# Kernel tuning notes

Measured on AMD Instinct MI355X. Metric: run time of the kernel, lower is better.

## Reference

```python
import jax, jax.numpy as jnp
import numpy as np

STRIDES = (128, 64, 32, 16, 8)
FM_SHAPES = ((6, 10), (12, 20), (24, 40), (48, 80), (96, 160))
RATIOS = np.array([1.0, 2.0, 3.0])
BASE_SIZE = 4
POS_THR, NEG_THR, IGNORE = 0.5, 0.4, -1.0
ALPHA, GAMMA, SIGMA = 0.25, 2.0, 3.0


def _cell_anchors(stride):
    # classic generate_anchors: base 4x4 anchor, 3 aspect ratios, scale=stride
    w = h = float(BASE_SIZE)
    ctr = (BASE_SIZE - 1) / 2.0
    size = w * h
    ws = np.round(np.sqrt(size / RATIOS))
    hs = np.round(ws * RATIOS)
    a = np.stack([ctr - 0.5 * (ws - 1), ctr - 0.5 * (hs - 1),
                  ctr + 0.5 * (ws - 1), ctr + 0.5 * (hs - 1)], 1)
    aw = a[:, 2] - a[:, 0] + 1
    ah = a[:, 3] - a[:, 1] + 1
    cx = a[:, 0] + 0.5 * (aw - 1)
    cy = a[:, 1] + 0.5 * (ah - 1)
    sw = aw * stride
    sh = ah * stride
    return np.stack([cx - 0.5 * (sw - 1), cy - 0.5 * (sh - 1),
                     cx + 0.5 * (sw - 1), cy + 0.5 * (sh - 1)], 1)


def _all_anchors():
    outs = []
    for (h, w), s in zip(FM_SHAPES, STRIDES):
        cell = _cell_anchors(s)  # [3,4]
        sx = np.tile((np.arange(w) * s)[None, :], (h, 1)).reshape(-1)
        sy = np.tile((np.arange(h) * s)[:, None], (1, w)).reshape(-1)
        shifts = np.stack([sx, sy, sx, sy], 1)  # [h*w,4]
        outs.append((cell[None] + shifts[:, None]).reshape(-1, 4))
    return np.concatenate(outs, 0).astype(np.float32)  # [A,4]


def box_overlap(b, g):
    ab = (b[:, 2] - b[:, 0] + 1) * (b[:, 3] - b[:, 1] + 1)
    ag = (g[:, 2] - g[:, 0] + 1) * (g[:, 3] - g[:, 1] + 1)
    iw = jnp.clip(jnp.minimum(b[:, None, 2], g[None, :, 2]) - jnp.maximum(b[:, None, 0], g[None, :, 0]) + 1, 0)
    ih = jnp.clip(jnp.minimum(b[:, None, 3], g[None, :, 3]) - jnp.maximum(b[:, None, 1], g[None, :, 1]) + 1, 0)
    inter = iw * ih
    return inter / (ab[:, None] + ag[None, :] - inter)


def bbox_transform_inv(anc, dlt):
    w = anc[..., 2] - anc[..., 0] + 1
    h = anc[..., 3] - anc[..., 1] + 1
    cx = anc[..., 0] + 0.5 * (w - 1)
    cy = anc[..., 1] + 0.5 * (h - 1)
    mx = jnp.log(jnp.asarray(1000.0 / 16, dlt.dtype))
    pw = jnp.exp(jnp.minimum(dlt[..., 2], mx)) * w
    ph = jnp.exp(jnp.minimum(dlt[..., 3], mx)) * h
    pcx = dlt[..., 0] * w + cx
    pcy = dlt[..., 1] * h + cy
    return jnp.stack([pcx - 0.5 * (pw - 1), pcy - 0.5 * (ph - 1),
                      pcx + 0.5 * (pw - 1), pcy + 0.5 * (ph - 1)], -1)


def bbox_transform(anc, gt):
    aw = anc[..., 2] - anc[..., 0] + 1
    ah = anc[..., 3] - anc[..., 1] + 1
    acx = anc[..., 0] + 0.5 * (aw - 1)
    acy = anc[..., 1] + 0.5 * (ah - 1)
    gw = gt[..., 2] - gt[..., 0] + 1
    gh = gt[..., 3] - gt[..., 1] + 1
    gcx = gt[..., 0] + 0.5 * (gw - 1)
    gcy = gt[..., 1] + 0.5 * (gh - 1)
    return jnp.stack([(gcx - acx) / aw, (gcy - acy) / ah,
                      jnp.log(gw / aw), jnp.log(gh / ah)], -1)


def conv3x3(x, w, b):
    y = jax.lax.conv_general_dilated(x, w, (1, 1), 'SAME',
                                     dimension_numbers=('NCHW', 'OIHW', 'NCHW'))
    return y + b[None, :, None, None]


def _head(feat, cls_w, cls_b, box_w, box_b, score_w, score_b,
          bpred_w, bpred_b, iou_w, iou_b, num_w, num_b):
    n = feat.shape[0]
    c = feat
    for i in range(4):
        c = jax.nn.relu(conv3x3(c, cls_w[i], cls_b[i]))
    cls_prob = jax.nn.sigmoid(conv3x3(c, score_w, score_b))
    num_prob = conv3x3(c, num_w, num_b)
    r = feat
    for i in range(4):
        r = jax.nn.relu(conv3x3(r, box_w[i], box_b[i]))
    offsets = conv3x3(r, bpred_w, bpred_b)
    iou_prob = conv3x3(r, iou_w, iou_b)
    rs = lambda t, ch: t.transpose(0, 2, 3, 1).reshape(n, -1, ch)
    return rs(cls_prob, 2), rs(num_prob, 2), rs(offsets, 8), rs(iou_prob, 2)


def _forward(feats, gt_boxes, im_info, cls_w, cls_b, box_w, box_b,
             score_w, score_b, bpred_w, bpred_b, iou_w, iou_b, num_w, num_b):
    outs = [_head(f, cls_w, cls_b, box_w, box_b, score_w, score_b,
                  bpred_w, bpred_b, iou_w, iou_b, num_w, num_b) for f in feats]
    cls_prob = jnp.concatenate([o[0] for o in outs], 1)  # [n,A,2]
    num_prob = jnp.concatenate([o[1] for o in outs], 1)  # [n,A,2]
    offsets = jnp.concatenate([o[2] for o in outs], 1)   # [n,A,8]
    iou_prob = jnp.concatenate([o[3] for o in outs], 1)  # [n,A,2]
    anchors = jnp.asarray(_all_anchors())                # [A,4]
    A = anchors.shape[0]
    n = cls_prob.shape[0]
    G = gt_boxes.shape[1]
    counts = im_info[:, 5]
    gidx = jnp.arange(G, dtype=jnp.float32)

    def anchor_target_one(gt, cnt):
        valid = (gidx < cnt) & (gt[:, 4] != IGNORE)
        ov = jnp.where(valid[None, :], box_overlap(anchors, gt[:, :4]), -1.0)
        top2, idx = jax.lax.top_k(ov, 2)  # [A,2]
        labels = jnp.where(top2 >= POS_THR, 1.0,
                           jnp.where(top2 < NEG_THR, 0.0, -1.0))
        tgt = bbox_transform(anchors[:, None, :], gt[idx, :4])  # [A,2,4]
        return labels, tgt.reshape(-1, 4)

    rpn_labels, target_boxes = jax.vmap(anchor_target_one)(gt_boxes, counts)
    rpn_labels = jax.lax.stop_gradient(rpn_labels)        # [n,A,2]
    target_boxes = jax.lax.stop_gradient(target_boxes)    # [n,2A,4]
    anchors2 = jnp.repeat(anchors, 2, axis=0)             # [2A,4] interleaved

    def iou_target_one(gt, cnt, off):
        dt = bbox_transform_inv(anchors2, off.reshape(-1, 4))  # [2A,4]
        keep = ((gidx < cnt) & (gt[:, 4] != IGNORE)).astype(dt.dtype)
        ov = box_overlap(dt, gt[:, :4]) * keep[None, :]        # [2A,G]
        ov = ov.reshape(A, 2, G)
        a, b = ov[:, 0], ov[:, 1]
        i1 = jnp.argmax(a, 1)
        av = jnp.take_along_axis(a, i1[:, None], 1)
        b = b.at[jnp.arange(A), i1].set(0.0)
        bv = jnp.max(b, 1, keepdims=True)
        return jnp.concatenate([av, bv], 1)                    # [A,2]

    ious_target = jax.lax.stop_gradient(
        jax.vmap(iou_target_one)(gt_boxes, counts, offsets))

    a, b = rpn_labels[..., 0], rpn_labels[..., 1]
    ignores = b - (a == 0).astype(b.dtype) * (b != 0).astype(b.dtype)
    labels = jnp.stack([a, ignores], 2).reshape(n, -1)     # [n,2A]

    # focal (sigmoid_cross_entropy_retina)
    p = cls_prob.reshape(n, -1, 1)                          # [n,2A,1]
    mask = (labels != IGNORE).astype(p.dtype)
    onehot = ((labels * mask) == 1).astype(p.dtype)[..., None]
    pos = (1 - p) ** GAMMA * onehot * jnp.log(p)
    neg = p ** GAMMA * (1 - onehot) * jnp.log(1 - p)
    npos = jnp.maximum((labels > 0).astype(p.dtype).sum(), 1.0)
    cls_loss = (-(ALPHA * pos + (1 - ALPHA) * neg).sum(-1) * mask).sum() / npos

    # smooth_l1_loss_retina (sigma=3)
    off4 = offsets.reshape(n, -1, 4)                        # [n,2A,4]
    diff = off4 - target_boxes
    ad = jnp.abs(diff)
    s2 = SIGMA * SIGMA
    sl1 = jnp.where(ad < 1.0 / s2, 0.5 * s2 * diff * diff, ad - 0.5 / s2)
    posm = (labels > 0).astype(off4.dtype)
    bbox_loss = (sl1.sum(-1) * posm).sum() / jnp.maximum(posm.sum(), 1.0)

    # iou_l1_loss
    lab2 = labels.reshape(n, -1, 2)                         # [n,A,2]
    ioumask = (lab2 > 0).astype(iou_prob.dtype)
    iou_loss = (jnp.abs(iou_prob.reshape(n, -1, 2) - ious_target) * ioumask).sum() \
        / jnp.maximum(ioumask.sum(), 1.0)

    # softmax_loss over num-per-anchor predictions
    nlabels = (lab2 > 0).sum(2).reshape(-1) - 1             # [n*A] in {-1,0,1}
    score = num_prob.reshape(-1, 2)
    logp = jax.nn.log_softmax(score, -1)
    nm = (nlabels != -1)
    vl = jnp.where(nm, nlabels, 0)
    nmf = nm.astype(score.dtype)
    num_loss = (-(jnp.take_along_axis(logp, vl[:, None], 1)[:, 0]) * nmf).sum() \
        / jnp.maximum(nmf.sum(), 1.0)

    return jnp.stack([cls_loss, 2.0 * bbox_loss, 2.0 * iou_loss, num_loss])


def setup_inputs() -> dict:
    key = jax.random.key(0)
    ks = jax.random.split(key, 24)
    n, G = 2, 32
    inp = {}
    for i, (h, w) in enumerate(FM_SHAPES):
        inp[f"feat_p{7 - i}"] = jax.random.normal(ks[i], (n, 256, h, w), jnp.float32) * 0.5
    x1 = jax.random.uniform(ks[5], (n, G), minval=0.0, maxval=900.0)
    y1 = jax.random.uniform(ks[6], (n, G), minval=0.0, maxval=500.0)
    bw = jax.random.uniform(ks[7], (n, G), minval=32.0, maxval=300.0)
    bh = jax.random.uniform(ks[8], (n, G), minval=32.0, maxval=300.0)
    inp["gt_boxes"] = jnp.stack([x1, y1, x1 + bw, y1 + bh, jnp.ones((n, G))], -1).astype(jnp.float32)
    inp["im_info"] = jnp.tile(jnp.array([[768., 1280., 1., 768., 1280., 24.]], jnp.float32), (n, 1))
    std = 0.01
    inp["cls_w"] = jax.random.normal(ks[9], (4, 256, 256, 3, 3), jnp.float32) * std
    inp["cls_b"] = jnp.zeros((4, 256), jnp.float32)
    inp["box_w"] = jax.random.normal(ks[10], (4, 256, 256, 3, 3), jnp.float32) * std
    inp["box_b"] = jnp.zeros((4, 256), jnp.float32)
    prior_bias = -float(np.log((1 - 0.01) / 0.01))
    inp["score_w"] = jax.random.normal(ks[11], (6, 256, 3, 3), jnp.float32) * std
    inp["score_b"] = jnp.full((6,), prior_bias, jnp.float32)
    inp["bpred_w"] = jax.random.normal(ks[12], (24, 256, 3, 3), jnp.float32) * std
    inp["bpred_b"] = jnp.zeros((24,), jnp.float32)
    inp["iou_w"] = jax.random.normal(ks[13], (6, 256, 3, 3), jnp.float32) * std
    inp["iou_b"] = jnp.zeros((6,), jnp.float32)
    inp["num_w"] = jax.random.normal(ks[14], (6, 256, 3, 3), jnp.float32) * std
    inp["num_b"] = jnp.zeros((6,), jnp.float32)
    return inp


def reference(feat_p7, feat_p6, feat_p5, feat_p4, feat_p3, gt_boxes, im_info,
              cls_w, cls_b, box_w, box_b, score_w, score_b, bpred_w, bpred_b,
              iou_w, iou_b, num_w, num_b):
    feats = [feat_p7, feat_p6, feat_p5, feat_p4, feat_p3]
    return _forward(feats, gt_boxes, im_info, cls_w, cls_b, box_w, box_b,
                    score_w, score_b, bpred_w, bpred_b, iou_w, iou_b, num_w, num_b)
```

## Files before the change

### kernel.cpp

```cpp
#include <hip/hip_runtime.h>
#include <math.h>

#define A_TOTAL 61380
#define NGT 32

typedef _Float16 f16;
typedef f16 f16x8 __attribute__((ext_vector_type(8)));
typedef float f32x4 __attribute__((ext_vector_type(4)));

__device__ __constant__ int LV_H[5]    = {6, 12, 24, 48, 96};
__device__ __constant__ int LV_W[5]    = {10, 20, 40, 80, 160};
__device__ __constant__ int LV_BASE[5] = {0, 60, 300, 1260, 5100};
__device__ __constant__ int LV_TX[5]   = {1, 2, 3, 5, 10};

typedef __attribute__((address_space(1))) const void* gptr_t;
typedef __attribute__((address_space(3))) void* lptr_t;
__device__ __forceinline__ void cp16_g2l(const void* g, void* l) {
  __builtin_amdgcn_global_load_lds((gptr_t)g, (lptr_t)l, 16, 0, 0);
}

__device__ __forceinline__ void get_tile8(int t, int& lv, int& y0, int& x0)
{
  int local;
  if (t >= 44)      { lv = 4; local = t - 44; }
  else if (t >= 14) { lv = 3; local = t - 14; }
  else if (t >= 5)  { lv = 2; local = t - 5; }
  else if (t >= 1)  { lv = 1; local = t - 1; }
  else              { lv = 0; local = 0; }
  int tX = LV_TX[lv];
  y0 = (local / tX) * 8;
  x0 = (local % tX) * 16;
}

__device__ __forceinline__ void get_tile16(int t, int& lv, int& y0, int& x0)
{
  int local;
  if (t >= 24)      { lv = 4; local = t - 24; }
  else if (t >= 9)  { lv = 3; local = t - 9; }
  else if (t >= 3)  { lv = 2; local = t - 3; }
  else if (t >= 1)  { lv = 1; local = t - 1; }
  else              { lv = 0; local = 0; }
  int tX = LV_TX[lv];
  y0 = (local / tX) * 16;
  x0 = (local % tX) * 16;
}

__global__ __launch_bounds__(256) void feats_to_nhwc(
    const float* __restrict__ f0, const float* __restrict__ f1,
    const float* __restrict__ f2, const float* __restrict__ f3,
    const float* __restrict__ f4, f16* __restrict__ act)
{
  const int b = blockIdx.z;
  const int c0 = blockIdx.y * 32;
  const int p0 = blockIdx.x * 32;
  const int tx = threadIdx.x & 31, ty = threadIdx.x >> 5;
  __shared__ float tl[32][33];

  int p = p0 + tx;
  const float* src = f0; int po = 0, HW = 60;
  if (p >= 5100)      { src = f4; po = p - 5100; HW = 15360; }
  else if (p >= 1260) { src = f3; po = p - 1260; HW = 3840; }
  else if (p >= 300)  { src = f2; po = p - 300;  HW = 960; }
  else if (p >= 60)   { src = f1; po = p - 60;   HW = 240; }
  else                { src = f0; po = p;        HW = 60; }

#pragma unroll
  for (int k = 0; k < 4; ++k) {
    int c = c0 + ty + k * 8;
    float v = 0.f;
    if (p < 20460) v = src[((size_t)b * 256 + c) * HW + po];
    tl[ty + k * 8][tx] = v;
  }
  __syncthreads();
#pragma unroll
  for (int k = 0; k < 4; ++k) {
    int pp = p0 + ty + k * 8;
    if (pp < 20460)
      act[((size_t)b * 20460 + pp) * 256 + c0 + tx] = (f16)tl[tx][ty + k * 8];
  }
}

__global__ __launch_bounds__(256) void prep_tower_w3(
    const float* __restrict__ cls_w, const float* __restrict__ box_w,
    f16* __restrict__ wT)
{
  int blk = blockIdx.x;
  int l = blk >> 8, co = blk & 255;
  const float* src = (l < 4 ? cls_w + (size_t)l * 589824
                            : box_w + (size_t)(l - 4) * 589824)
                   + (size_t)co * 2304;
  __shared__ f16 sm[2304];
  int t = threadIdx.x;
#pragma unroll
  for (int j = 0; j < 9; ++j) sm[t + j * 256] = (f16)src[t + j * 256];
  __syncthreads();
#pragma unroll
  for (int it = 0; it < 2; ++it) {
    int c = t + it * 256;
    if (c < 288) {
      int tap = c >> 5, s = c & 31;
      f16x8 v;
#pragma unroll
      for (int e = 0; e < 8; ++e) v[e] = sm[(s * 8 + e) * 9 + tap];
      *(f16x8*)(wT + ((((size_t)l * 9 + tap) * 32 + s) * 256 + co) * 8) = v;
    }
  }
}

__global__ void prep_head_w3(const float* __restrict__ sw, const float* __restrict__ nw,
                             const float* __restrict__ bw, const float* __restrict__ iw,
                             const float* __restrict__ sb, const float* __restrict__ nb2,
                             const float* __restrict__ bb, const float* __restrict__ ib,
                             f16* __restrict__ wH, float* __restrict__ hb)
{
  int idx = blockIdx.x * 256 + threadIdx.x;
  if (idx < 18432) {
    int p = idx / 9216, rem = idx - p * 9216;
    int tap = rem / 1024, rem2 = rem - tap * 1024;
    int s = rem2 >> 5, co = rem2 & 31;
    int C1 = p ? 24 : 6;
    const float* w1 = p ? bw : sw;
    const float* w2 = p ? iw : nw;
    f16x8 v;
#pragma unroll
    for (int e = 0; e < 8; ++e) {
      int ci = s * 8 + e;
      float x = 0.f;
      if (co < C1)          x = w1[((size_t)co * 256 + ci) * 9 + tap];
      else if (co < C1 + 6) x = w2[((size_t)(co - C1) * 256 + ci) * 9 + tap];
      v[e] = (f16)x;
    }
    *(f16x8*)(wH + (size_t)idx * 8) = v;
  }
  if (idx < 64) {
    int pp = idx >> 5, jj = idx & 31;
    int C1b = pp ? 24 : 6;
    const float* b1 = pp ? bb : sb;
    const float* b2 = pp ? ib : nb2;
    float bv = 0.f;
    if (jj < C1b)          bv = b1[jj];
    else if (jj < C1b + 6) bv = b2[jj - C1b];
    hb[idx] = bv;
  }
}

__global__ __launch_bounds__(256, 2) void conv_mfma_tower2(
    const f16* __restrict__ in_cls, f16* __restrict__ out_cls,
    const f16* __restrict__ in_box, f16* __restrict__ out_box,
    const f16* __restrict__ wT, const float* __restrict__ cls_b,
    const float* __restrict__ box_b, int layer)
{
  int lv, y0, x0;
  get_tile8(blockIdx.x, lv, y0, x0);
  const int H = LV_H[lv], W = LV_W[lv], base = LV_BASE[lv];
  const int b = blockIdx.y, tw = blockIdx.z;
  const f16* in  = tw ? in_box : in_cls;
  f16*       out = tw ? out_box : out_cls;
  const f16* wB = wT + (size_t)(tw * 4 + layer) * 2304 * 256;
  const float* bias = (tw ? box_b : cls_b) + layer * 256;

  const int tid = threadIdx.x;
  const int lane = tid & 63, wid = tid >> 6;
  const int m = lane & 15, q = lane >> 4;
  const int mrow = (wid & 1) * 4;
  const int ncol = (wid >> 1) * 128;

  __shared__ __align__(16) f16 Al[720 * 8];
  __shared__ __align__(16) f16 Bl[2 * 1024 * 8];

  f32x4 acc[4][8];
#pragma unroll
  for (int i = 0; i < 4; ++i)
#pragma unroll
    for (int j = 0; j < 8; ++j) acc[i][j] = (f32x4){0.f, 0.f, 0.f, 0.f};

  const f16* inb = in + (size_t)(b * 20460 + base) * 256;

  auto stageA = [&](int cb) {
#pragma unroll
    for (int it = 0; it < 3; ++it) {
      int u = tid + it * 256;
      if (u < 720) {
        int r = u / 72, rem = u - r * 72;
        int seg = rem / 18, px = rem - seg * 18;
        int gy = y0 - 1 + r, gx = x0 - 1 + px;
        uint4 v = {0, 0, 0, 0};
        if (gy >= 0 && gy < H && gx >= 0 && gx < W)
          v = *(const uint4*)(inb + (size_t)(gy * W + gx) * 256 + cb * 32 + seg * 8);
        *(uint4*)(Al + (size_t)u * 8) = v;
      }
    }
  };
  auto prefetchB = [&](int cb, int tap, int bsel) {
    const f16* wsrc = wB + (((size_t)tap * 32 + cb * 4) * 256) * 8;
    f16* dst = Bl + (size_t)bsel * 1024 * 8;
#pragma unroll
    for (int it = 0; it < 4; ++it) {
      int u = tid + it * 256;
      cp16_g2l(wsrc + (size_t)u * 8, dst + (size_t)u * 8);
    }
  };

  prefetchB(0, 0, 0);
  int buf = 0;
  for (int cb = 0; cb < 8; ++cb) {
    __syncthreads();
    stageA(cb);
    for (int tap = 0; tap < 9; ++tap) {
      __syncthreads();
      {
        int ncb = cb, ntap = tap + 1;
        if (ntap == 9) { ntap = 0; ncb++; }
        if (ncb < 8) prefetchB(ncb, ntap, buf ^ 1);
      }
      const int ky = tap / 3, kx = tap - ky * 3;
      f16x8 af[4];
#pragma unroll
      for (int mb = 0; mb < 4; ++mb)
        af[mb] = *(const f16x8*)(Al + (size_t)(((mrow + mb + ky) * 4 + q) * 18 + m + kx) * 8);
#pragma unroll
      for (int half = 0; half < 2; ++half) {
        f16x8 bf[4];
#pragma unroll
        for (int nb = 0; nb < 4; ++nb)
          bf[nb] = *(const f16x8*)(Bl + (size_t)(buf * 1024 + q * 256 + ncol + half * 64 + nb * 16 + m) * 8);
#pragma unroll
        for (int mb = 0; mb < 4; ++mb)
#pragma unroll
          for (int nb = 0; nb < 4; ++nb)
            acc[mb][half * 4 + nb] =
                __builtin_amdgcn_mfma_f32_16x16x32_f16(af[mb], bf[nb], acc[mb][half * 4 + nb], 0, 0, 0);
      }
      buf ^= 1;
    }
  }

#pragma unroll
  for (int mb = 0; mb < 4; ++mb) {
    int y = y0 + mrow + mb;
    if (y >= H) continue;
#pragma unroll
    for (int nb = 0; nb < 8; ++nb) {
      int co = ncol + nb * 16 + m;
      float bi = bias[co];
#pragma unroll
      for (int r = 0; r < 4; ++r) {
        int x = x0 + q * 4 + r;
        if (x < W) {
          float v = fmaxf(acc[mb][nb][r] + bi, 0.f);
          out[(size_t)(b * 20460 + base + y * W + x) * 256 + co] = (f16)v;
        }
      }
    }
  }
}

__global__ __launch_bounds__(256) void conv_mfma_head2(
    const f16* __restrict__ in_cls, const f16* __restrict__ in_box,
    const f16* __restrict__ wH, const float* __restrict__ hb,
    float* __restrict__ cls_prob, float* __restrict__ num_prob,
    float* __restrict__ offsets, float* __restrict__ iou_prob)
{
  int lv, y0, x0;
  get_tile16(blockIdx.x, lv, y0, x0);
  const int H = LV_H[lv], W = LV_W[lv], base = LV_BASE[lv];
  const int b = blockIdx.y, z = blockIdx.z;
  const f16* in = z ? in_box : in_cls;
  const f16* wB = wH + (size_t)z * 2304 * 32;
  const float* hbz = hb + z * 32;
  float* o1 = z ? offsets : cls_prob;
  float* o2 = z ? iou_prob : num_prob;
  const int C1 = z ? 24 : 6, P1 = z ? 8 : 2, SIG = z ? 0 : 1;

  const int tid = threadIdx.x;
  const int lane = tid & 63, wid = tid >> 6;
  const int m = lane & 15, q = lane >> 4;

  __shared__ __align__(16) f16 Al[1296 * 8];
  __shared__ __align__(16) f16 Bl[2 * 128 * 8];

  f32x4 acc[4][2];
#pragma unroll
  for (int i = 0; i < 4; ++i) { acc[i][0] = (f32x4){0,0,0,0}; acc[i][1] = (f32x4){0,0,0,0}; }

  const f16* inb = in + (size_t)(b * 20460 + base) * 256;

  auto prefetchB = [&](int cb, int tap, int bsel) {
    if (tid < 128) {
      const f16* wsrc = wB + (((size_t)tap * 32 + cb * 4) * 32) * 8;
      cp16_g2l(wsrc + (size_t)tid * 8, Bl + (size_t)(bsel * 128 + tid) * 8);
    }
  };

  prefetchB(0, 0, 0);
  int buf = 0;
  for (int cb = 0; cb < 8; ++cb) {
    __syncthreads();
#pragma unroll
    for (int it = 0; it < 6; ++it) {
      int u = tid + it * 256;
      if (u < 1296) {
        int r = u / 72, rem = u - r * 72;
        int seg = rem / 18, px = rem - seg * 18;
        int gy = y0 - 1 + r, gx = x0 - 1 + px;
        uint4 v = {0, 0, 0, 0};
        if (gy >= 0 && gy < H && gx >= 0 && gx < W)
          v = *(const uint4*)(inb + (size_t)(gy * W + gx) * 256 + cb * 32 + seg * 8);
        *(uint4*)(Al + (size_t)u * 8) = v;
      }
    }
    for (int tap = 0; tap < 9; ++tap) {
      __syncthreads();
      {
        int ncb = cb, ntap = tap + 1;
        if (ntap == 9) { ntap = 0; ncb++; }
        if (ncb < 8) prefetchB(ncb, ntap, buf ^ 1);
      }
      const int ky = tap / 3, kx = tap - ky * 3;
      f16x8 af[4], bf[2];
#pragma unroll
      for (int mb = 0; mb < 4; ++mb)
        af[mb] = *(const f16x8*)(Al + (size_t)(((wid * 4 + mb + ky) * 4 + q) * 18 + m + kx) * 8);
#pragma unroll
      for (int nb = 0; nb < 2; ++nb)
        bf[nb] = *(const f16x8*)(Bl + (size_t)(buf * 128 + q * 32 + nb * 16 + m) * 8);
#pragma unroll
      for (int mb = 0; mb < 4; ++mb)
#pragma unroll
        for (int nb = 0; nb < 2; ++nb)
          acc[mb][nb] = __builtin_amdgcn_mfma_f32_16x16x32_f16(af[mb], bf[nb], acc[mb][nb], 0, 0, 0);
      buf ^= 1;
    }
  }

  const int ro = base * 3;
#pragma unroll
  for (int mb = 0; mb < 4; ++mb) {
    int y = y0 + wid * 4 + mb;
    if (y >= H) continue;
#pragma unroll
    for (int nb = 0; nb < 2; ++nb) {
      int j = nb * 16 + m;
      if (j >= C1 + 6) continue;
      float bi = hbz[j];
#pragma unroll
      for (int r = 0; r < 4; ++r) {
        int x = x0 + q * 4 + r;
        if (x < W) {
          float v = acc[mb][nb][r] + bi;
          int row0 = ro + (y * W + x) * 3;
          if (j < C1) {
            if (SIG) v = 1.f / (1.f + expf(-v));
            int jd = j / P1;
            o1[((size_t)b * A_TOTAL + row0 + jd) * P1 + (j - jd * P1)] = v;
          } else {
            int jj = j - C1;
            o2[((size_t)b * A_TOTAL + row0 + (jj >> 1)) * 2 + (jj & 1)] = v;
          }
        }
      }
    }
  }
}

__global__ void gen_anchors(float* __restrict__ anchors)
{
  int i = blockIdx.x * 256 + threadIdx.x;
  if (i >= A_TOTAL) return;
  int off, s, Wl;
  if (i >= 15300)     { off = 15300; s = 8;   Wl = 160; }
  else if (i >= 3780) { off = 3780;  s = 16;  Wl = 80;  }
  else if (i >= 900)  { off = 900;   s = 32;  Wl = 40;  }
  else if (i >= 180)  { off = 180;   s = 64;  Wl = 20;  }
  else                { off = 0;     s = 128; Wl = 10;  }
  int r = i - off;
  int cell = r / 3, a = r - cell * 3;
  int y = cell / Wl, x = cell - y * Wl;
  float wsv = (a == 0) ? 4.f : (a == 1) ? 3.f : 2.f;
  float hsv = (a == 0) ? 4.f : 6.f;
  float sw = wsv * (float)s, sh = hsv * (float)s;
  float cx = (float)(x * s) + 1.5f, cy = (float)(y * s) + 1.5f;
  anchors[i * 4 + 0] = cx - 0.5f * (sw - 1.f);
  anchors[i * 4 + 1] = cy - 0.5f * (sh - 1.f);
  anchors[i * 4 + 2] = cx + 0.5f * (sw - 1.f);
  anchors[i * 4 + 3] = cy + 0.5f * (sh - 1.f);
}

__global__ __launch_bounds__(256) void anchor_target(
    const float* __restrict__ anchors, const float* __restrict__ gt,
    const float* __restrict__ iminfo, float* __restrict__ rpn, float* __restrict__ tgt)
{
  int i = blockIdx.x * 256 + threadIdx.x;
  int b = blockIdx.y;
  if (i >= A_TOTAL) return;
  float cnt = iminfo[b * 6 + 5];
  float ax1 = anchors[i*4+0], ay1 = anchors[i*4+1], ax2 = anchors[i*4+2], ay2 = anchors[i*4+3];
  float aw = ax2 - ax1 + 1.f, ah = ay2 - ay1 + 1.f, ab = aw * ah;
  float v1 = -1e30f, v2 = -1e30f; int i1 = 0, i2 = 0;
  for (int g = 0; g < NGT; ++g) {
    const float* gp = gt + (b * NGT + g) * 5;
    float ov = -1.f;
    if ((float)g < cnt && gp[4] != -1.f) {
      float iw = fmaxf(fminf(ax2, gp[2]) - fmaxf(ax1, gp[0]) + 1.f, 0.f);
      float ih = fmaxf(fminf(ay2, gp[3]) - fmaxf(ay1, gp[1]) + 1.f, 0.f);
      float inter = iw * ih;
      float ag = (gp[2] - gp[0] + 1.f) * (gp[3] - gp[1] + 1.f);
      ov = inter / (ab + ag - inter);
    }
    if (ov > v1)      { v2 = v1; i2 = i1; v1 = ov; i1 = g; }
    else if (ov > v2) { v2 = ov; i2 = g; }
  }
  float l1 = (v1 >= 0.5f) ? 1.f : ((v1 < 0.4f) ? 0.f : -1.f);
  float l2 = (v2 >= 0.5f) ? 1.f : ((v2 < 0.4f) ? 0.f : -1.f);
  rpn[(b * A_TOTAL + i) * 2 + 0] = l1;
  rpn[(b * A_TOTAL + i) * 2 + 1] = l2;
  float acx = ax1 + 0.5f * (aw - 1.f), acy = ay1 + 0.5f * (ah - 1.f);
  int idx2[2] = {i1, i2};
#pragma unroll
  for (int k = 0; k < 2; ++k) {
    const float* gp = gt + (b * NGT + idx2[k]) * 5;
    float gw = gp[2] - gp[0] + 1.f, gh = gp[3] - gp[1] + 1.f;
    float gcx = gp[0] + 0.5f * (gw - 1.f), gcy = gp[1] + 0.5f * (gh - 1.f);
    float* o = tgt + ((size_t)(b * 2 * A_TOTAL) + i * 2 + k) * 4;
    o[0] = (gcx - acx) / aw;  o[1] = (gcy - acy) / ah;
    o[2] = logf(gw / aw);     o[3] = logf(gh / ah);
  }
}

__global__ __launch_bounds__(256) void iou_target(
    const float* __restrict__ anchors, const float* __restrict__ gt,
    const float* __restrict__ iminfo, const float* __restrict__ offsets,
    float* __restrict__ ioust)
{
  int i = blockIdx.x * 256 + threadIdx.x;
  int b = blockIdx.y;
  if (i >= A_TOTAL) return;
  float cnt = iminfo[b * 6 + 5];
  float ax1 = anchors[i*4+0], ay1 = anchors[i*4+1], ax2 = anchors[i*4+2], ay2 = anchors[i*4+3];
  float aw = ax2 - ax1 + 1.f, ah = ay2 - ay1 + 1.f;
  float acx = ax1 + 0.5f * (aw - 1.f), acy = ay1 + 0.5f * (ah - 1.f);
  const float mx = 4.135166556742356f;
  float bx[2][4];
#pragma unroll
  for (int k = 0; k < 2; ++k) {
    const float* d = offsets + ((size_t)(b * A_TOTAL) + i) * 8 + k * 4;
    float pw = expf(fminf(d[2], mx)) * aw;
    float ph = expf(fminf(d[3], mx)) * ah;
    float pcx = d[0] * aw + acx, pcy = d[1] * ah + acy;
    bx[k][0] = pcx - 0.5f * (pw - 1.f); bx[k][1] = pcy - 0.5f * (ph - 1.f);
    bx[k][2] = pcx + 0.5f * (pw - 1.f); bx[k][3] = pcy + 0.5f * (ph - 1.f);
  }
  float area0 = (bx[0][2]-bx[0][0]+1.f) * (bx[0][3]-bx[0][1]+1.f);
  float area1 = (bx[1][2]-bx[1][0]+1.f) * (bx[1][3]-bx[1][1]+1.f);
  float av = -1e30f; int i1 = 0;
  for (int g = 0; g < NGT; ++g) {
    const float* gp = gt + (b * NGT + g) * 5;
    float keep = ((float)g < cnt && gp[4] != -1.f) ? 1.f : 0.f;
    float ag = (gp[2] - gp[0] + 1.f) * (gp[3] - gp[1] + 1.f);
    float iw = fmaxf(fminf(bx[0][2], gp[2]) - fmaxf(bx[0][0], gp[0]) + 1.f, 0.f);
    float ih = fmaxf(fminf(bx[0][3], gp[3]) - fmaxf(bx[0][1], gp[1]) + 1.f, 0.f);
    float inter = iw * ih;
    float ov = inter / (area0 + ag - inter) * keep;
    if (ov > av) { av = ov; i1 = g; }
  }
  float bv = -1e30f;
  for (int g = 0; g < NGT; ++g) {
    float val = 0.f;
    if (g != i1) {
      const float* gp = gt + (b * NGT + g) * 5;
      float keep = ((float)g < cnt && gp[4] != -1.f) ? 1.f : 0.f;
      float ag = (gp[2] - gp[0] + 1.f) * (gp[3] - gp[1] + 1.f);
      float iw = fmaxf(fminf(bx[1][2], gp[2]) - fmaxf(bx[1][0], gp[0]) + 1.f, 0.f);
      float ih = fmaxf(fminf(bx[1][3], gp[3]) - fmaxf(bx[1][1], gp[1]) + 1.f, 0.f);
      float inter = iw * ih;
      val = inter / (area1 + ag - inter) * keep;
    }
    bv = fmaxf(bv, val);
  }
  ioust[(b * A_TOTAL + i) * 2 + 0] = av;
  ioust[(b * A_TOTAL + i) * 2 + 1] = bv;
}

__global__ __launch_bounds__(256) void loss_reduce(
    const float* __restrict__ cls_prob, const float* __restrict__ num_prob,
    const float* __restrict__ offsets,  const float* __restrict__ iou_prob,
    const float* __restrict__ rpn,      const float* __restrict__ tgt,
    const float* __restrict__ ioust,    float* __restrict__ accum)
{
  int i = blockIdx.x * 256 + threadIdx.x;
  int b = blockIdx.y;
  float cls_s = 0.f, npos = 0.f, bb_s = 0.f, iou_s = 0.f, num_s = 0.f, num_c = 0.f;
  float la = 0.f, ign = 0.f;
  if (i < A_TOTAL) {
    int base = b * A_TOTAL + i;
    la = rpn[base * 2 + 0];
    float lb = rpn[base * 2 + 1];
    ign = lb - ((la == 0.f && lb != 0.f) ? 1.f : 0.f);
    float lab2[2] = {la, ign};
#pragma unroll
    for (int j = 0; j < 2; ++j) {
      float l = lab2[j];
      float mask = (l != -1.f) ? 1.f : 0.f;
      bool oh = (l * mask) == 1.f;
      float p = cls_prob[base * 2 + j];
      float term = oh ? (0.25f * (1.f - p) * (1.f - p) * logf(p))
                      : (0.75f * p * p * logf(1.f - p));
      cls_s += -term * mask;
      if (l > 0.f) {
        npos += 1.f;
#pragma unroll
        for (int c = 0; c < 4; ++c) {
          float d = offsets[(size_t)base * 8 + j * 4 + c]
                  - tgt[((size_t)(b * 2 * A_TOTAL) + i * 2 + j) * 4 + c];
          float ad = fabsf(d);
          bb_s += (ad < 1.f / 9.f) ? (4.5f * d * d) : (ad - 0.5f / 9.f);
        }
        iou_s += fabsf(iou_prob[base * 2 + j] - ioust[base * 2 + j]);
      }
    }
    int nl = ((la > 0.f) ? 1 : 0) + ((ign > 0.f) ? 1 : 0) - 1;
    if (nl != -1) {
      float s0 = num_prob[base * 2], s1 = num_prob[base * 2 + 1];
      float mm = fmaxf(s0, s1);
      float lse = mm + logf(expf(s0 - mm) + expf(s1 - mm));
      num_s += lse - ((nl == 0) ? s0 : s1);
      num_c += 1.f;
    }
  }
  __shared__ float red[6][4];
  float vals[6] = {cls_s, npos, bb_s, iou_s, num_s, num_c};
  int lane = threadIdx.x & 63, wid = threadIdx.x >> 6;
#pragma unroll
  for (int qq = 0; qq < 6; ++qq) {
    float v = vals[qq];
#pragma unroll
    for (int o = 32; o > 0; o >>= 1) v += __shfl_down(v, o);
    if (lane == 0) red[qq][wid] = v;
  }
  __syncthreads();
  if (threadIdx.x < 6) {
    float s = red[threadIdx.x][0] + red[threadIdx.x][1] + red[threadIdx.x][2] + red[threadIdx.x][3];
    atomicAdd(&accum[threadIdx.x], s);
  }
}

__global__ void finalize_loss(const float* __restrict__ acc, float* __restrict__ out)
{
  float npos = fmaxf(acc[1], 1.f);
  out[0] = acc[0] / npos;
  out[1] = 2.f * acc[2] / npos;
  out[2] = 2.f * acc[3] / npos;
  out[3] = acc[4] / fmaxf(acc[5], 1.f);
}

extern "C" void kernel_launch(void* const* d_in, const int* in_sizes, int n_in,
                              void* d_out, int out_size, void* d_ws, size_t ws_size,
                              hipStream_t stream)
{
  (void)in_sizes; (void)n_in; (void)out_size; (void)ws_size;
  const float* feat[5];
  for (int i = 0; i < 5; ++i) feat[i] = (const float*)d_in[i];
  const float* gt      = (const float*)d_in[5];
  const float* iminfo  = (const float*)d_in[6];
  const float* cls_w   = (const float*)d_in[7];
  const float* cls_b   = (const float*)d_in[8];
  const float* box_w   = (const float*)d_in[9];
  const float* box_b   = (const float*)d_in[10];
  const float* score_w = (const float*)d_in[11];
  const float* score_b = (const float*)d_in[12];
  const float* bpred_w = (const float*)d_in[13];
  const float* bpred_b = (const float*)d_in[14];
  const float* iou_w   = (const float*)d_in[15];
  const float* iou_b   = (const float*)d_in[16];
  const float* num_w   = (const float*)d_in[17];
  const float* num_b   = (const float*)d_in[18];

  const size_t ACT = (size_t)2 * 20460 * 256;
  f16* actF = (f16*)d_ws;
  f16* actA = actF + ACT;
  f16* actB = actA + ACT;
  f16* actC = actB + ACT;
  f16* wT   = actC + ACT;
  f16* wH   = wT + (size_t)8 * 2304 * 256;
  float* hb = (float*)(wH + (size_t)2 * 2304 * 32);

  float* cls_prob = (float*)actA;
  float* num_prob = cls_prob + 2 * A_TOTAL * 2;
  float* offsets  = num_prob + 2 * A_TOTAL * 2;
  float* iou_prob = offsets + 2 * A_TOTAL * 8;
  float* anchors  = iou_prob + 2 * A_TOTAL * 2;
  float* rpn      = anchors + A_TOTAL * 4;
  float* tgt      = rpn + 2 * A_TOTAL * 2;
  float* ioust    = tgt + 2 * 2 * A_TOTAL * 4;
  float* accum    = ioust + 2 * A_TOTAL * 2;

  prep_tower_w3<<<dim3(2048), 256, 0, stream>>>(cls_w, box_w, wT);
  prep_head_w3<<<dim3(72), 256, 0, stream>>>(
      score_w, num_w, bpred_w, iou_w, score_b, num_b, bpred_b, iou_b, wH, hb);
  feats_to_nhwc<<<dim3(640, 8, 2), 256, 0, stream>>>(
      feat[0], feat[1], feat[2], feat[3], feat[4], actF);

  dim3 tg(164, 2, 2);
  conv_mfma_tower2<<<tg, 256, 0, stream>>>(actF, actA, actF, actC, wT, cls_b, box_b, 0);
  conv_mfma_tower2<<<tg, 256, 0, stream>>>(actA, actB, actC, actF, wT, cls_b, box_b, 1);
  conv_mfma_tower2<<<tg, 256, 0, stream>>>(actB, actA, actF, actC, wT, cls_b, box_b, 2);
  conv_mfma_tower2<<<tg, 256, 0, stream>>>(actA, actB, actC, actF, wT, cls_b, box_b, 3);

  conv_mfma_head2<<<dim3(84, 2, 2), 256, 0, stream>>>(
      actB, actF, wH, hb, cls_prob, num_prob, offsets, iou_prob);

  hipMemsetAsync(accum, 0, 8 * sizeof(float), stream);
  dim3 agrid((A_TOTAL + 255) / 256, 2);
  gen_anchors<<<dim3((A_TOTAL + 255) / 256), 256, 0, stream>>>(anchors);
  anchor_target<<<agrid, 256, 0, stream>>>(anchors, gt, iminfo, rpn, tgt);
  iou_target<<<agrid, 256, 0, stream>>>(anchors, gt, iminfo, offsets, ioust);
  loss_reduce<<<agrid, 256, 0, stream>>>(cls_prob, num_prob, offsets, iou_prob,
                                         rpn, tgt, ioust, accum);
  finalize_loss<<<1, 1, 0, stream>>>(accum, (float*)d_out);
}
```

Measured before the change: 877.7 us.

## Pad activations with zero borders and load conv operands directly from global

Activations are stored in a spatially padded NHWC layout. A new kernel zeroes the one-pixel border, so the tower and head convolutions no longer need bounds checks on input. With that, the conv kernels drop LDS staging, the async weight prefetch and every __syncthreads, and each wave reads A and B fragments straight from global memory through the caches. The memset of the loss accumulator is also folded into gen_anchors. The aim is to remove barrier and staging overhead, at the risk of losing LDS data reuse and exposing global-load latency to the MFMA loop.

```diff
diff --git a/kernel.cpp b/kernel.cpp
--- a/kernel.cpp
+++ b/kernel.cpp
@@ -3,6 +3,7 @@
 
 #define A_TOTAL 61380
 #define NGT 32
+#define PTOT 21472
 
 typedef _Float16 f16;
 typedef f16 f16x8 __attribute__((ext_vector_type(8)));
@@ -10,14 +11,8 @@
 
 __device__ __constant__ int LV_H[5]    = {6, 12, 24, 48, 96};
 __device__ __constant__ int LV_W[5]    = {10, 20, 40, 80, 160};
-__device__ __constant__ int LV_BASE[5] = {0, 60, 300, 1260, 5100};
+__device__ __constant__ int LV_PB[5]   = {0, 96, 404, 1496, 5596};
 __device__ __constant__ int LV_TX[5]   = {1, 2, 3, 5, 10};
-
-typedef __attribute__((address_space(1))) const void* gptr_t;
-typedef __attribute__((address_space(3))) void* lptr_t;
-__device__ __forceinline__ void cp16_g2l(const void* g, void* l) {
-  __builtin_amdgcn_global_load_lds((gptr_t)g, (lptr_t)l, 16, 0, 0);
-}
 
 __device__ __forceinline__ void get_tile8(int t, int& lv, int& y0, int& x0)
 {
@@ -45,6 +40,34 @@
   x0 = (local % tX) * 16;
 }
 
+__device__ __forceinline__ int padded_off(int p)
+{
+  if (p >= 5100)      { int po = p - 5100; int y = po / 160, x = po - y * 160; return 5596 + (y + 1) * 162 + x + 1; }
+  else if (p >= 1260) { int po = p - 1260; int y = po / 80,  x = po - y * 80;  return 1496 + (y + 1) * 82  + x + 1; }
+  else if (p >= 300)  { int po = p - 300;  int y = po / 40,  x = po - y * 40;  return 404  + (y + 1) * 42  + x + 1; }
+  else if (p >= 60)   { int po = p - 60;   int y = po / 20,  x = po - y * 20;  return 96   + (y + 1) * 22  + x + 1; }
+  else                { int y = p / 10, x = p - y * 10;                         return (y + 1) * 12 + x + 1; }
+}
+
+__global__ __launch_bounds__(64) void zero_borders(f16* __restrict__ act)
+{
+  int e = blockIdx.x, b = blockIdx.y, z = blockIdx.z;
+  int lv, e0;
+  if (e >= 496)      { lv = 4; e0 = e - 496; }
+  else if (e >= 236) { lv = 3; e0 = e - 236; }
+  else if (e >= 104) { lv = 2; e0 = e - 104; }
+  else if (e >= 36)  { lv = 1; e0 = e - 36; }
+  else               { lv = 0; e0 = e; }
+  int Hp = LV_H[lv] + 2, Wp = LV_W[lv] + 2;
+  int y, x;
+  if (e0 < Wp)          { y = 0;      x = e0; }
+  else if (e0 < 2 * Wp) { y = Hp - 1; x = e0 - Wp; }
+  else { int e2 = e0 - 2 * Wp; y = 1 + (e2 >> 1); x = (e2 & 1) ? (Wp - 1) : 0; }
+  f16* dst = act + ((size_t)z * 2 * PTOT + (size_t)b * PTOT + LV_PB[lv] + y * Wp + x) * 256
+           + threadIdx.x * 4;
+  *(uint2*)dst = (uint2){0u, 0u};
+}
+
 __global__ __launch_bounds__(256) void feats_to_nhwc(
     const float* __restrict__ f0, const float* __restrict__ f1,
     const float* __restrict__ f2, const float* __restrict__ f3,
@@ -57,12 +80,13 @@
   __shared__ float tl[32][33];
 
   int p = p0 + tx;
-  const float* src = f0; int po = 0, HW = 60;
-  if (p >= 5100)      { src = f4; po = p - 5100; HW = 15360; }
-  else if (p >= 1260) { src = f3; po = p - 1260; HW = 3840; }
-  else if (p >= 300)  { src = f2; po = p - 300;  HW = 960; }
-  else if (p >= 60)   { src = f1; po = p - 60;   HW = 240; }
-  else                { src = f0; po = p;        HW = 60; }
+  const float* src = f0; int po = 0;
+  if (p >= 5100)      { src = f4; po = p - 5100; }
+  else if (p >= 1260) { src = f3; po = p - 1260; }
+  else if (p >= 300)  { src = f2; po = p - 300;  }
+  else if (p >= 60)   { src = f1; po = p - 60;   }
+  else                { src = f0; po = p;        }
+  int HW = (p >= 5100) ? 15360 : (p >= 1260) ? 3840 : (p >= 300) ? 960 : (p >= 60) ? 240 : 60;
 
 #pragma unroll
   for (int k = 0; k < 4; ++k) {
@@ -76,7 +100,7 @@
   for (int k = 0; k < 4; ++k) {
     int pp = p0 + ty + k * 8;
     if (pp < 20460)
-      act[((size_t)b * 20460 + pp) * 256 + c0 + tx] = (f16)tl[tx][ty + k * 8];
+      act[((size_t)b * PTOT + padded_off(pp)) * 256 + c0 + tx] = (f16)tl[tx][ty + k * 8];
   }
 }
 
@@ -144,7 +168,7 @@
   }
 }
 
-__global__ __launch_bounds__(256, 2) void conv_mfma_tower2(
+__global__ __launch_bounds__(256, 2) void conv_mfma_tower3(
     const f16* __restrict__ in_cls, f16* __restrict__ out_cls,
     const f16* __restrict__ in_box, f16* __restrict__ out_box,
     const f16* __restrict__ wT, const float* __restrict__ cls_b,
@@ -152,7 +176,7 @@
 {
   int lv, y0, x0;
   get_tile8(blockIdx.x, lv, y0, x0);
-  const int H = LV_H[lv], W = LV_W[lv], base = LV_BASE[lv];
+  const int H = LV_H[lv], W = LV_W[lv], Wp = W + 2, pbase = LV_PB[lv];
   const int b = blockIdx.y, tw = blockIdx.z;
   const f16* in  = tw ? in_box : in_cls;
   f16*       out = tw ? out_box : out_cls;
@@ -165,76 +189,38 @@
   const int mrow = (wid & 1) * 4;
   const int ncol = (wid >> 1) * 128;
 
-  __shared__ __align__(16) f16 Al[720 * 8];
-  __shared__ __align__(16) f16 Bl[2 * 1024 * 8];
-
   f32x4 acc[4][8];
 #pragma unroll
   for (int i = 0; i < 4; ++i)
 #pragma unroll
     for (int j = 0; j < 8; ++j) acc[i][j] = (f32x4){0.f, 0.f, 0.f, 0.f};
 
-  const f16* inb = in + (size_t)(b * 20460 + base) * 256;
-
-  auto stageA = [&](int cb) {
-#pragma unroll
-    for (int it = 0; it < 3; ++it) {
-      int u = tid + it * 256;
-      if (u < 720) {
-        int r = u / 72, rem = u - r * 72;
-        int seg = rem / 18, px = rem - seg * 18;
-        int gy = y0 - 1 + r, gx = x0 - 1 + px;
-        uint4 v = {0, 0, 0, 0};
-        if (gy >= 0 && gy < H && gx >= 0 && gx < W)
-          v = *(const uint4*)(inb + (size_t)(gy * W + gx) * 256 + cb * 32 + seg * 8);
-        *(uint4*)(Al + (size_t)u * 8) = v;
-      }
-    }
-  };
-  auto prefetchB = [&](int cb, int tap, int bsel) {
-    const f16* wsrc = wB + (((size_t)tap * 32 + cb * 4) * 256) * 8;
-    f16* dst = Bl + (size_t)bsel * 1024 * 8;
-#pragma unroll
-    for (int it = 0; it < 4; ++it) {
-      int u = tid + it * 256;
-      cp16_g2l(wsrc + (size_t)u * 8, dst + (size_t)u * 8);
-    }
-  };
-
-  prefetchB(0, 0, 0);
-  int buf = 0;
+  const f16* inb = in + (size_t)(b * PTOT + pbase) * 256;
+  const f16* pA = inb + ((size_t)(y0 + mrow) * Wp + x0 + m) * 256 + q * 8;
+  const f16* pB = wB + ((size_t)q * 256 + ncol + m) * 8;
+
   for (int cb = 0; cb < 8; ++cb) {
-    __syncthreads();
-    stageA(cb);
+    const f16* pAc = pA + cb * 32;
+    const f16* pBc = pB + (size_t)cb * 4 * 256 * 8;
+#pragma unroll
     for (int tap = 0; tap < 9; ++tap) {
-      __syncthreads();
-      {
-        int ncb = cb, ntap = tap + 1;
-        if (ntap == 9) { ntap = 0; ncb++; }
-        if (ncb < 8) prefetchB(ncb, ntap, buf ^ 1);
-      }
       const int ky = tap / 3, kx = tap - ky * 3;
-      f16x8 af[4];
+      f16x8 af[4], bf[8];
 #pragma unroll
       for (int mb = 0; mb < 4; ++mb)
-        af[mb] = *(const f16x8*)(Al + (size_t)(((mrow + mb + ky) * 4 + q) * 18 + m + kx) * 8);
-#pragma unroll
-      for (int half = 0; half < 2; ++half) {
-        f16x8 bf[4];
-#pragma unroll
-        for (int nb = 0; nb < 4; ++nb)
-          bf[nb] = *(const f16x8*)(Bl + (size_t)(buf * 1024 + q * 256 + ncol + half * 64 + nb * 16 + m) * 8);
-#pragma unroll
-        for (int mb = 0; mb < 4; ++mb)
-#pragma unroll
-          for (int nb = 0; nb < 4; ++nb)
-            acc[mb][half * 4 + nb] =
-                __builtin_amdgcn_mfma_f32_16x16x32_f16(af[mb], bf[nb], acc[mb][half * 4 + nb], 0, 0, 0);
-      }
-      buf ^= 1;
-    }
-  }
-
+        af[mb] = *(const f16x8*)(pAc + ((size_t)(mb + ky) * Wp + kx) * 256);
+#pragma unroll
+      for (int nb = 0; nb < 8; ++nb)
+        bf[nb] = *(const f16x8*)(pBc + (size_t)tap * 65536 + nb * 128);
+#pragma unroll
+      for (int mb = 0; mb < 4; ++mb)
+#pragma unroll
+        for (int nb = 0; nb < 8; ++nb)
+          acc[mb][nb] = __builtin_amdgcn_mfma_f32_16x16x32_f16(af[mb], bf[nb], acc[mb][nb], 0, 0, 0);
+    }
+  }
+
+  f16* outb = out + (size_t)(b * PTOT + pbase) * 256;
 #pragma unroll
   for (int mb = 0; mb < 4; ++mb) {
     int y = y0 + mrow + mb;
@@ -248,14 +234,14 @@
         int x = x0 + q * 4 + r;
         if (x < W) {
           float v = fmaxf(acc[mb][nb][r] + bi, 0.f);
-          out[(size_t)(b * 20460 + base + y * W + x) * 256 + co] = (f16)v;
+          outb[((size_t)(y + 1) * Wp + x + 1) * 256 + co] = (f16)v;
         }
       }
     }
   }
 }
 
-__global__ __launch_bounds__(256) void conv_mfma_head2(
+__global__ __launch_bounds__(256) void conv_mfma_head3(
     const f16* __restrict__ in_cls, const f16* __restrict__ in_box,
     const f16* __restrict__ wH, const float* __restrict__ hb,
     float* __restrict__ cls_prob, float* __restrict__ num_prob,
@@ -263,7 +249,7 @@
 {
   int lv, y0, x0;
   get_tile16(blockIdx.x, lv, y0, x0);
-  const int H = LV_H[lv], W = LV_W[lv], base = LV_BASE[lv];
+  const int H = LV_H[lv], W = LV_W[lv], Wp = W + 2, pbase = LV_PB[lv];
   const int b = blockIdx.y, z = blockIdx.z;
   const f16* in = z ? in_box : in_cls;
   const f16* wB = wH + (size_t)z * 2304 * 32;
@@ -276,64 +262,37 @@
   const int lane = tid & 63, wid = tid >> 6;
   const int m = lane & 15, q = lane >> 4;
 
-  __shared__ __align__(16) f16 Al[1296 * 8];
-  __shared__ __align__(16) f16 Bl[2 * 128 * 8];
-
   f32x4 acc[4][2];
 #pragma unroll
   for (int i = 0; i < 4; ++i) { acc[i][0] = (f32x4){0,0,0,0}; acc[i][1] = (f32x4){0,0,0,0}; }
 
-  const f16* inb = in + (size_t)(b * 20460 + base) * 256;
-
-  auto prefetchB = [&](int cb, int tap, int bsel) {
-    if (tid < 128) {
-      const f16* wsrc = wB + (((size_t)tap * 32 + cb * 4) * 32) * 8;
-      cp16_g2l(wsrc + (size_t)tid * 8, Bl + (size_t)(bsel * 128 + tid) * 8);
-    }
-  };
-
-  prefetchB(0, 0, 0);
-  int buf = 0;
+  const f16* inb = in + (size_t)(b * PTOT + pbase) * 256;
+  const f16* pA = inb + ((size_t)(y0 + wid * 4) * Wp + x0 + m) * 256 + q * 8;
+  const f16* pB = wB + ((size_t)q * 32 + m) * 8;
+
   for (int cb = 0; cb < 8; ++cb) {
-    __syncthreads();
-#pragma unroll
-    for (int it = 0; it < 6; ++it) {
-      int u = tid + it * 256;
-      if (u < 1296) {
-        int r = u / 72, rem = u - r * 72;
-        int seg = rem / 18, px = rem - seg * 18;
-        int gy = y0 - 1 + r, gx = x0 - 1 + px;
-        uint4 v = {0, 0, 0, 0};
-        if (gy >= 0 && gy < H && gx >= 0 && gx < W)
-          v = *(const uint4*)(inb + (size_t)(gy * W + gx) * 256 + cb * 32 + seg * 8);
-        *(uint4*)(Al + (size_t)u * 8) = v;
-      }
-    }
+    const f16* pAc = pA + cb * 32;
+    const f16* pBc = pB + (size_t)cb * 4 * 32 * 8;
+#pragma unroll
     for (int tap = 0; tap < 9; ++tap) {
-      __syncthreads();
-      {
-        int ncb = cb, ntap = tap + 1;
-        if (ntap == 9) { ntap = 0; ncb++; }
-        if (ncb < 8) prefetchB(ncb, ntap, buf ^ 1);
-      }
       const int ky = tap / 3, kx = tap - ky * 3;
       f16x8 af[4], bf[2];
 #pragma unroll
       for (int mb = 0; mb < 4; ++mb)
-        af[mb] = *(const f16x8*)(Al + (size_t)(((wid * 4 + mb + ky) * 4 + q) * 18 + m + kx) * 8);
+        af[mb] = *(const f16x8*)(pAc + ((size_t)(mb + ky) * Wp + kx) * 256);
 #pragma unroll
       for (int nb = 0; nb < 2; ++nb)
-        bf[nb] = *(const f16x8*)(Bl + (size_t)(buf * 128 + q * 32 + nb * 16 + m) * 8);
+        bf[nb] = *(const f16x8*)(pBc + (size_t)tap * 8192 + nb * 128);
 #pragma unroll
       for (int mb = 0; mb < 4; ++mb)
 #pragma unroll
         for (int nb = 0; nb < 2; ++nb)
           acc[mb][nb] = __builtin_amdgcn_mfma_f32_16x16x32_f16(af[mb], bf[nb], acc[mb][nb], 0, 0, 0);
-      buf ^= 1;
-    }
-  }
-
-  const int ro = base * 3;
+    }
+  }
+
+  const int ro = pbase * 0 + 0;
+  const int robase = (lv == 0 ? 0 : lv == 1 ? 60 : lv == 2 ? 300 : lv == 3 ? 1260 : 5100) * 3;
 #pragma unroll
   for (int mb = 0; mb < 4; ++mb) {
     int y = y0 + wid * 4 + mb;
@@ -348,7 +307,7 @@
         int x = x0 + q * 4 + r;
         if (x < W) {
           float v = acc[mb][nb][r] + bi;
-          int row0 = ro + (y * W + x) * 3;
+          int row0 = robase + (y * W + x) * 3;
           if (j < C1) {
             if (SIG) v = 1.f / (1.f + expf(-v));
             int jd = j / P1;
@@ -361,11 +320,13 @@
       }
     }
   }
-}
-
-__global__ void gen_anchors(float* __restrict__ anchors)
+  (void)ro;
+}
+
+__global__ void gen_anchors(float* __restrict__ anchors, float* __restrict__ accum)
 {
   int i = blockIdx.x * 256 + threadIdx.x;
+  if (blockIdx.x == 0 && threadIdx.x < 8) accum[threadIdx.x] = 0.f;
   if (i >= A_TOTAL) return;
   int off, s, Wl;
   if (i >= 15300)     { off = 15300; s = 8;   Wl = 160; }
@@ -575,12 +536,12 @@
   const float* num_w   = (const float*)d_in[17];
   const float* num_b   = (const float*)d_in[18];
 
-  const size_t ACT = (size_t)2 * 20460 * 256;
+  const size_t ACT2 = (size_t)2 * PTOT * 256;
   f16* actF = (f16*)d_ws;
-  f16* actA = actF + ACT;
-  f16* actB = actA + ACT;
-  f16* actC = actB + ACT;
-  f16* wT   = actC + ACT;
+  f16* actA = actF + ACT2;
+  f16* actB = actA + ACT2;
+  f16* actC = actB + ACT2;
+  f16* wT   = actC + ACT2;
   f16* wH   = wT + (size_t)8 * 2304 * 256;
   float* hb = (float*)(wH + (size_t)2 * 2304 * 32);
 
@@ -597,21 +558,21 @@
   prep_tower_w3<<<dim3(2048), 256, 0, stream>>>(cls_w, box_w, wT);
   prep_head_w3<<<dim3(72), 256, 0, stream>>>(
       score_w, num_w, bpred_w, iou_w, score_b, num_b, bpred_b, iou_b, wH, hb);
+  zero_borders<<<dim3(1012, 2, 4), 64, 0, stream>>>(actF);
   feats_to_nhwc<<<dim3(640, 8, 2), 256, 0, stream>>>(
       feat[0], feat[1], feat[2], feat[3], feat[4], actF);
 
   dim3 tg(164, 2, 2);
-  conv_mfma_tower2<<<tg, 256, 0, stream>>>(actF, actA, actF, actC, wT, cls_b, box_b, 0);
-  conv_mfma_tower2<<<tg, 256, 0, stream>>>(actA, actB, actC, actF, wT, cls_b, box_b, 1);
-  conv_mfma_tower2<<<tg, 256, 0, stream>>>(actB, actA, actF, actC, wT, cls_b, box_b, 2);
-  conv_mfma_tower2<<<tg, 256, 0, stream>>>(actA, actB, actC, actF, wT, cls_b, box_b, 3);
-
-  conv_mfma_head2<<<dim3(84, 2, 2), 256, 0, stream>>>(
+  conv_mfma_tower3<<<tg, 256, 0, stream>>>(actF, actA, actF, actC, wT, cls_b, box_b, 0);
+  conv_mfma_tower3<<<tg, 256, 0, stream>>>(actA, actB, actC, actF, wT, cls_b, box_b, 1);
+  conv_mfma_tower3<<<tg, 256, 0, stream>>>(actB, actA, actF, actC, wT, cls_b, box_b, 2);
+  conv_mfma_tower3<<<tg, 256, 0, stream>>>(actA, actB, actC, actF, wT, cls_b, box_b, 3);
+
+  conv_mfma_head3<<<dim3(84, 2, 2), 256, 0, stream>>>(
       actB, actF, wH, hb, cls_prob, num_prob, offsets, iou_prob);
 
-  hipMemsetAsync(accum, 0, 8 * sizeof(float), stream);
   dim3 agrid((A_TOTAL + 255) / 256, 2);
-  gen_anchors<<<dim3((A_TOTAL + 255) / 256), 256, 0, stream>>>(anchors);
+  gen_anchors<<<dim3((A_TOTAL + 255) / 256), 256, 0, stream>>>(anchors, accum);
   anchor_target<<<agrid, 256, 0, stream>>>(anchors, gt, iminfo, rpn, tgt);
   iou_target<<<agrid, 256, 0, stream>>>(anchors, gt, iminfo, offsets, ioust);
   loss_reduce<<<agrid, 256, 0, stream>>>(cls_prob, num_prob, offsets, iou_prob,
```

New measurement: 842.0 us. 1.04x faster.
